# Optimization experiments

Hardware: AMD Instinct MI355X
Metric: run time of the kernel (lower is better)

The kernel has to match this reference:

```python
import jax, jax.numpy as jnp
import numpy as np

B = 8          # number of scenes in batch
N_PER = 4096   # points per scene (equal-sized contiguous batches)
C_IN = 64
C_OUT = 128
RATIO = 0.25
K = 32
EPS = 1e-5


def setup_inputs() -> dict:
    key = jax.random.key(0)
    ks = jax.random.split(key, 10)
    N = B * N_PER
    x = jax.random.normal(ks[0], (N, C_IN), dtype=jnp.float32)
    pos = jax.random.uniform(ks[1], (N, 3), dtype=jnp.float32)
    batch = jnp.repeat(jnp.arange(B, dtype=jnp.int64), N_PER)
    d_in = C_IN + 3
    s1 = 1.0 / np.sqrt(d_in)
    s2 = 1.0 / np.sqrt(C_OUT)
    W1 = jax.random.uniform(ks[2], (d_in, C_OUT), jnp.float32, -s1, s1)
    b1 = jax.random.uniform(ks[3], (C_OUT,), jnp.float32, -s1, s1)
    g1 = jnp.ones((C_OUT,), jnp.float32)
    be1 = jnp.zeros((C_OUT,), jnp.float32)
    W2 = jax.random.uniform(ks[4], (C_OUT, C_OUT), jnp.float32, -s2, s2)
    b2 = jax.random.uniform(ks[5], (C_OUT,), jnp.float32, -s2, s2)
    g2 = jnp.ones((C_OUT,), jnp.float32)
    be2 = jnp.zeros((C_OUT,), jnp.float32)
    return {"x": x, "pos": pos, "batch": batch, "W1": W1, "b1": b1,
            "g1": g1, "be1": be1, "W2": W2, "b2": b2, "g2": g2, "be2": be2}


def _ln(y, g, b):
    mu = y.mean(-1, keepdims=True)
    v = ((y - mu) ** 2).mean(-1, keepdims=True)
    return (y - mu) * jax.lax.rsqrt(v + EPS) * g + b


def reference(x, pos, batch, W1, b1, g1, be1, W2, b2, g2, be2):
    N, C = x.shape
    n = N_PER
    m = int(n * RATIO)  # samples per scene
    xb = x.reshape(B, n, C)
    posb = pos.reshape(B, n, 3)
    # deterministic sampling: first m points of each (randomly generated) scene
    pos_down = posb[:, :m]  # (B, m, 3)
    # squared euclidean distances (same ordering as cdist for topk/argmin)
    d2 = jnp.sum((pos_down[:, :, None, :] - posb[:, None, :, :]) ** 2, axis=-1)  # (B,m,n)
    _, knn_idx = jax.lax.top_k(-d2, K)  # (B, m, K), k smallest distances
    bidx = jnp.arange(B)[:, None, None]
    knn_feat = xb[bidx, knn_idx]       # (B, m, K, C)
    knn_pos = posb[bidx, knn_idx]      # (B, m, K, 3)
    rel_pos = knn_pos - pos_down[:, :, None, :]
    h = jnp.concatenate([knn_feat, rel_pos], axis=-1)  # (B, m, K, C+3)
    h = jax.nn.gelu(_ln(h @ W1 + b1, g1, be1), approximate=False)
    h = jax.nn.gelu(_ln(h @ W2 + b2, g2, be2), approximate=False)
    x_down = h.max(axis=2).reshape(B * m, -1)          # (M, C_OUT)
    pos_down_flat = pos_down.reshape(B * m, 3)
    batch_down = jnp.repeat(jnp.arange(B, dtype=batch.dtype), m)
    # nearest downsampled point for each original point (for upsampling)
    d2u = jnp.sum((posb[:, :, None, :] - pos_down[:, None, :, :]) ** 2, axis=-1)  # (B,n,m)
    nearest = jnp.argmin(d2u, axis=-1)                 # (B, n), local index
    upsample_idx = (nearest + jnp.arange(B)[:, None] * m).reshape(N)
    return x_down, pos_down_flat, batch_down, upsample_idx
```

## Files before the change

### kernel.cpp

```cpp
#include <hip/hip_runtime.h>
#include <math.h>

#define NPER 4096
#define MDOWN 1024
#define KNNK 32
#define CIN 64
#define DIN 67
#define KPAD 96
#define SSTR 136

typedef _Float16 half8 __attribute__((ext_vector_type(8)));
typedef _Float16 half4 __attribute__((ext_vector_type(4)));
typedef float f32x4 __attribute__((ext_vector_type(4)));

#define SENTU 0xFFFFFFFFFFFFFFFFULL

__device__ __forceinline__ float d2f(float qx, float qy, float qz,
                                     float px, float py, float pz) {
    float dx = __fsub_rn(qx, px);
    float dy = __fsub_rn(qy, py);
    float dz = __fsub_rn(qz, pz);
    return __fadd_rn(__fadd_rn(__fmul_rn(dx, dx), __fmul_rn(dy, dy)), __fmul_rn(dz, dz));
}

__device__ __forceinline__ float gelu_f(float y) {
    return 0.5f * y * (1.0f + erff(y * 0.70710678118654752440f));
}

__device__ __forceinline__ void insert4(unsigned long long v,
                                        unsigned long long& t0, unsigned long long& t1,
                                        unsigned long long& t2, unsigned long long& t3) {
    if (v < t3) {
        unsigned long long m2 = t2 > v ? t2 : v;
        t3 = t3 < m2 ? t3 : m2;
        unsigned long long m1 = t1 > v ? t1 : v;
        t2 = t2 < m1 ? t2 : m1;
        unsigned long long m0 = t0 > v ? t0 : v;
        t1 = t1 < m0 ? t1 : m0;
        t0 = t0 < v ? t0 : v;
    }
}

__global__ __launch_bounds__(256) void prep_kernel(const float* __restrict__ W1,
                                                   const float* __restrict__ W2,
                                                   _Float16* __restrict__ W1t,
                                                   _Float16* __restrict__ W2t) {
    int t = blockIdx.x * 256 + threadIdx.x;
    if (t < 128 * KPAD) {
        int k = t >> 7, c = t & 127;
        float v = (k < DIN) ? W1[k * 128 + c] : 0.0f;
        W1t[(size_t)c * KPAD + k] = (_Float16)v;
    }
    int t2 = t - 128 * KPAD;
    if (t2 >= 0 && t2 < 128 * 128) {
        int k = t2 >> 7, c = t2 & 127;
        W2t[(size_t)c * 128 + k] = (_Float16)W2[t2];
    }
}

__global__ __launch_bounds__(256) void knn_kernel(const float* __restrict__ pos,
                                                  int* __restrict__ knn) {
    int tid = threadIdx.x;
    int lane = tid & 63;
    int q = blockIdx.x * 4 + (tid >> 6);
    int b = q >> 10;
    int i = q & 1023;
    const float* pb = pos + (size_t)b * NPER * 3;
    float qx = pb[i * 3], qy = pb[i * 3 + 1], qz = pb[i * 3 + 2];

    unsigned long long t0 = SENTU, t1 = SENTU, t2 = SENTU, t3 = SENTU;
    unsigned long long taken = 0ULL;

    #pragma unroll 4
    for (int s = 0; s < 64; ++s) {
        int j = s * 64 + lane;
        float d2 = d2f(qx, qy, qz, pb[j * 3], pb[j * 3 + 1], pb[j * 3 + 2]);
        unsigned long long v = ((unsigned long long)__float_as_uint(d2) << 32) | (unsigned)j;
        insert4(v, t0, t1, t2, t3);
    }

    for (int r = 0; r < KNNK; ++r) {
        if (t0 == SENTU) {
            for (int s = 0; s < 64; ++s) {
                if (!((taken >> s) & 1ULL)) {
                    int j = s * 64 + lane;
                    float d2 = d2f(qx, qy, qz, pb[j * 3], pb[j * 3 + 1], pb[j * 3 + 2]);
                    unsigned long long v =
                        ((unsigned long long)__float_as_uint(d2) << 32) | (unsigned)j;
                    insert4(v, t0, t1, t2, t3);
                }
            }
        }
        unsigned long long w = t0;
        #pragma unroll
        for (int d = 1; d < 64; d <<= 1) {
            unsigned long long o = __shfl_xor(w, d, 64);
            w = o < w ? o : w;
        }
        if (t0 == w) {
            taken |= 1ULL << (((unsigned)(w & 0xFFFFFFFFu)) >> 6);
            t0 = t1; t1 = t2; t2 = t3; t3 = SENTU;
        }
        if (lane == 0) knn[q * KNNK + r] = (int)(unsigned)(w & 0xFFFFFFFFu);
    }
}

__global__ __launch_bounds__(512, 4) void mlp_kernel(
    const float* __restrict__ x, const float* __restrict__ pos,
    const int* __restrict__ knn,
    const _Float16* __restrict__ W1t, const _Float16* __restrict__ W2t,
    const float* __restrict__ b1, const float* __restrict__ g1, const float* __restrict__ be1,
    const float* __restrict__ b2, const float* __restrict__ g2, const float* __restrict__ be2,
    float* __restrict__ out0) {
    __shared__ __align__(16) _Float16 S[128][SSTR];
    __shared__ float pmax[8][128];
    __shared__ int jidx[128];
    __shared__ float qpos[4][3];

    int tid = threadIdx.x;
    int q0 = blockIdx.x * 4;
    int b = q0 >> 10;
    const float* pb = pos + (size_t)b * NPER * 3;

    if (tid < 128) jidx[tid] = knn[(q0 + (tid >> 5)) * KNNK + (tid & 31)];
    if (tid < 12) {
        int qq = tid / 3, comp = tid % 3;
        int iq = (q0 + qq) & 1023;
        qpos[qq][comp] = pb[iq * 3 + comp];
    }
    __syncthreads();

    for (int t = tid; t < 128 * 16; t += 512) {
        int r = t >> 4, c4 = (t & 15) * 4;
        int j = jidx[r];
        float4 v = *(const float4*)(x + ((size_t)(b * NPER + j)) * CIN + c4);
        half4 hv = {(_Float16)v.x, (_Float16)v.y, (_Float16)v.z, (_Float16)v.w};
        *(half4*)&S[r][c4] = hv;
    }
    for (int t = tid; t < 128 * 8; t += 512) {
        int r = t >> 3, k = t & 7;
        half4 hv = {(_Float16)0.f, (_Float16)0.f, (_Float16)0.f, (_Float16)0.f};
        if (k == 0) {
            int j = jidx[r];
            int qq = r >> 5;
            hv.x = (_Float16)__fsub_rn(pb[j * 3 + 0], qpos[qq][0]);
            hv.y = (_Float16)__fsub_rn(pb[j * 3 + 1], qpos[qq][1]);
            hv.z = (_Float16)__fsub_rn(pb[j * 3 + 2], qpos[qq][2]);
        }
        *(half4*)&S[r][64 + 4 * k] = hv;
    }
    __syncthreads();

    int lane = tid & 63, wid = tid >> 6;
    int c16 = lane & 15, g = lane >> 4;
    int r0 = wid * 16;

    f32x4 acc[8];
    #pragma unroll
    for (int n = 0; n < 8; ++n) acc[n] = (f32x4){0.f, 0.f, 0.f, 0.f};

    #pragma unroll
    for (int ks = 0; ks < 3; ++ks) {
        half8 a = *(const half8*)&S[r0 + c16][ks * 32 + 8 * g];
        #pragma unroll
        for (int n = 0; n < 8; ++n) {
            half8 bf = *(const half8*)(W1t + (size_t)(n * 16 + c16) * KPAD + ks * 32 + 8 * g);
            acc[n] = __builtin_amdgcn_mfma_f32_16x16x32_f16(a, bf, acc[n], 0, 0, 0);
        }
    }

    {
        float bv[8], gv[8], bev[8];
        #pragma unroll
        for (int n = 0; n < 8; ++n) {
            int c = n * 16 + c16;
            bv[n] = b1[c]; gv[n] = g1[c]; bev[n] = be1[c];
        }
        #pragma unroll
        for (int t = 0; t < 4; ++t) {
            float s = 0.f;
            #pragma unroll
            for (int n = 0; n < 8; ++n) { acc[n][t] += bv[n]; s += acc[n][t]; }
            s += __shfl_xor(s, 1, 64); s += __shfl_xor(s, 2, 64);
            s += __shfl_xor(s, 4, 64); s += __shfl_xor(s, 8, 64);
            float mu = s * (1.0f / 128.0f);
            float vv = 0.f;
            #pragma unroll
            for (int n = 0; n < 8; ++n) { float d = acc[n][t] - mu; vv += d * d; }
            vv += __shfl_xor(vv, 1, 64); vv += __shfl_xor(vv, 2, 64);
            vv += __shfl_xor(vv, 4, 64); vv += __shfl_xor(vv, 8, 64);
            float rstd = rsqrtf(vv * (1.0f / 128.0f) + 1e-5f);
            int row = r0 + 4 * g + t;
            #pragma unroll
            for (int n = 0; n < 8; ++n) {
                float z = (acc[n][t] - mu) * rstd;
                float y = z * gv[n] + bev[n];
                S[row][16 * n + c16] = (_Float16)gelu_f(y);
            }
        }
    }

    f32x4 acc2[8];
    #pragma unroll
    for (int n = 0; n < 8; ++n) acc2[n] = (f32x4){0.f, 0.f, 0.f, 0.f};

    #pragma unroll
    for (int ks = 0; ks < 4; ++ks) {
        half8 a = *(const half8*)&S[r0 + c16][ks * 32 + 8 * g];
        #pragma unroll
        for (int n = 0; n < 8; ++n) {
            half8 bf = *(const half8*)(W2t + (size_t)(n * 16 + c16) * 128 + ks * 32 + 8 * g);
            acc2[n] = __builtin_amdgcn_mfma_f32_16x16x32_f16(a, bf, acc2[n], 0, 0, 0);
        }
    }

    {
        float bv[8], gv[8], bev[8];
        #pragma unroll
        for (int n = 0; n < 8; ++n) {
            int c = n * 16 + c16;
            bv[n] = b2[c]; gv[n] = g2[c]; bev[n] = be2[c];
        }
        float mx[8];
        #pragma unroll
        for (int n = 0; n < 8; ++n) mx[n] = -3.4e38f;
        #pragma unroll
        for (int t = 0; t < 4; ++t) {
            float s = 0.f;
            #pragma unroll
            for (int n = 0; n < 8; ++n) { acc2[n][t] += bv[n]; s += acc2[n][t]; }
            s += __shfl_xor(s, 1, 64); s += __shfl_xor(s, 2, 64);
            s += __shfl_xor(s, 4, 64); s += __shfl_xor(s, 8, 64);
            float mu = s * (1.0f / 128.0f);
            float vv = 0.f;
            #pragma unroll
            for (int n = 0; n < 8; ++n) { float d = acc2[n][t] - mu; vv += d * d; }
            vv += __shfl_xor(vv, 1, 64); vv += __shfl_xor(vv, 2, 64);
            vv += __shfl_xor(vv, 4, 64); vv += __shfl_xor(vv, 8, 64);
            float rstd = rsqrtf(vv * (1.0f / 128.0f) + 1e-5f);
            #pragma unroll
            for (int n = 0; n < 8; ++n) {
                float z = (acc2[n][t] - mu) * rstd;
                float y = z * gv[n] + bev[n];
                float h = gelu_f(y);
                mx[n] = fmaxf(mx[n], h);
            }
        }
        #pragma unroll
        for (int n = 0; n < 8; ++n) {
            mx[n] = fmaxf(mx[n], __shfl_xor(mx[n], 16, 64));
            mx[n] = fmaxf(mx[n], __shfl_xor(mx[n], 32, 64));
        }
        if (lane < 16) {
            #pragma unroll
            for (int n = 0; n < 8; ++n) pmax[wid][n * 16 + c16] = mx[n];
        }
    }
    __syncthreads();

    {
        int q = tid >> 7, c = tid & 127;
        out0[(size_t)(q0 + q) * 128 + c] = fmaxf(pmax[2 * q][c], pmax[2 * q + 1][c]);
    }
}

__global__ __launch_bounds__(256) void up_kernel(const float* __restrict__ pos,
                                                 float* __restrict__ out1,
                                                 float* __restrict__ out2,
                                                 float* __restrict__ out3) {
    int b = blockIdx.x >> 6, jb = blockIdx.x & 63;
    __shared__ float pd[3072];
    __shared__ unsigned long long red[192];
    int tid = threadIdx.x;
    const float* pb = pos + (size_t)b * NPER * 3;
    for (int t = tid; t < 3072; t += 256) pd[t] = pb[t];
    __syncthreads();

    int qlane = tid & 63;
    int part = tid >> 6;
    int j = jb * 64 + qlane;
    float qx = pb[j * 3], qy = pb[j * 3 + 1], qz = pb[j * 3 + 2];
    unsigned long long best = SENTU;
    int i0 = part * 256;
    #pragma unroll 4
    for (int i = i0; i < i0 + 256; ++i) {
        float d2 = d2f(qx, qy, qz, pd[i * 3], pd[i * 3 + 1], pd[i * 3 + 2]);
        unsigned long long v = ((unsigned long long)__float_as_uint(d2) << 32) | (unsigned)i;
        best = v < best ? v : best;
    }
    if (part > 0) red[(part - 1) * 64 + qlane] = best;
    __syncthreads();
    if (part == 0) {
        unsigned long long o0 = red[qlane];
        unsigned long long o1 = red[64 + qlane];
        unsigned long long o2 = red[128 + qlane];
        best = o0 < best ? o0 : best;
        best = o1 < best ? o1 : best;
        best = o2 < best ? o2 : best;
        int ii = (int)(unsigned)(best & 0xFFFFFFFFu);
        out3[(size_t)b * NPER + j] = (float)(ii + b * MDOWN);
    }
    if (jb == 0) {
        for (int t = tid; t < 3072; t += 256) out1[b * 3072 + t] = pd[t];
        for (int t = tid; t < 1024; t += 256) out2[b * 1024 + t] = (float)b;
    }
}

extern "C" void kernel_launch(void* const* d_in, const int* in_sizes, int n_in,
                              void* d_out, int out_size, void* d_ws, size_t ws_size,
                              hipStream_t stream) {
    const float* x   = (const float*)d_in[0];
    const float* pos = (const float*)d_in[1];
    const float* W1  = (const float*)d_in[3];
    const float* b1  = (const float*)d_in[4];
    const float* g1  = (const float*)d_in[5];
    const float* be1 = (const float*)d_in[6];
    const float* W2  = (const float*)d_in[7];
    const float* b2  = (const float*)d_in[8];
    const float* g2  = (const float*)d_in[9];
    const float* be2 = (const float*)d_in[10];

    float* out  = (float*)d_out;
    float* out0 = out;
    float* out1 = out + 1048576;
    float* out2 = out + 1048576 + 24576;
    float* out3 = out + 1048576 + 24576 + 8192;

    int* knn = (int*)d_ws;
    _Float16* W1t = (_Float16*)((char*)d_ws + 8192 * 32 * 4);
    _Float16* W2t = W1t + 128 * KPAD;

    prep_kernel<<<112, 256, 0, stream>>>(W1, W2, W1t, W2t);
    knn_kernel<<<2048, 256, 0, stream>>>(pos, knn);
    mlp_kernel<<<2048, 512, 0, stream>>>(x, pos, knn, W1t, W2t,
                                         b1, g1, be1, b2, g2, be2, out0);
    up_kernel<<<512, 256, 0, stream>>>(pos, out1, out2, out3);
}
```

Baseline: 295.9 us.

## Apply GELU only at neighbour min/max and use polynomial erf approximation

Because GELU is unimodal (decreasing then increasing), the max over neighbours of GELU(y) equals the larger of GELU at the min and max of y. The second layer now tracks per-channel min/max of the pre-activation and evaluates GELU twice per output instead of per neighbour. Separately, erff is replaced by an Abramowitz–Stegun rational approximation with fast exp, cheapening the first layer's GELU at a small accuracy cost. An extra shared array and more shuffles are added for the min tracking.

```diff
diff --git a/kernel.cpp b/kernel.cpp
--- a/kernel.cpp
+++ b/kernel.cpp
@@ -24,7 +24,18 @@
 }
 
 __device__ __forceinline__ float gelu_f(float y) {
-    return 0.5f * y * (1.0f + erff(y * 0.70710678118654752440f));
+    float x = y * 0.70710678118654752440f;
+    float ax = fabsf(x);
+    float t = __frcp_rn(__fmaf_rn(0.3275911f, ax, 1.0f));
+    float p = __fmaf_rn(1.061405429f, t, -1.453152027f);
+    p = __fmaf_rn(p, t, 1.421413741f);
+    p = __fmaf_rn(p, t, -0.284496736f);
+    p = __fmaf_rn(p, t, 0.254829592f);
+    p = p * t;
+    float e = __expf(-ax * ax);
+    float erfax = __fmaf_rn(-p, e, 1.0f);
+    float er = copysignf(erfax, x);
+    return 0.5f * y * (1.0f + er);
 }
 
 __device__ __forceinline__ void insert4(unsigned long long v,
@@ -113,7 +124,8 @@
     const float* __restrict__ b2, const float* __restrict__ g2, const float* __restrict__ be2,
     float* __restrict__ out0) {
     __shared__ __align__(16) _Float16 S[128][SSTR];
-    __shared__ float pmax[8][128];
+    __shared__ float pymx[8][128];
+    __shared__ float pymn[8][128];
     __shared__ int jidx[128];
     __shared__ float qpos[4][3];
 
@@ -221,9 +233,9 @@
             int c = n * 16 + c16;
             bv[n] = b2[c]; gv[n] = g2[c]; bev[n] = be2[c];
         }
-        float mx[8];
-        #pragma unroll
-        for (int n = 0; n < 8; ++n) mx[n] = -3.4e38f;
+        float ymx[8], ymn[8];
+        #pragma unroll
+        for (int n = 0; n < 8; ++n) { ymx[n] = -3.4e38f; ymn[n] = 3.4e38f; }
         #pragma unroll
         for (int t = 0; t < 4; ++t) {
             float s = 0.f;
@@ -242,25 +254,32 @@
             for (int n = 0; n < 8; ++n) {
                 float z = (acc2[n][t] - mu) * rstd;
                 float y = z * gv[n] + bev[n];
-                float h = gelu_f(y);
-                mx[n] = fmaxf(mx[n], h);
+                ymx[n] = fmaxf(ymx[n], y);
+                ymn[n] = fminf(ymn[n], y);
             }
         }
         #pragma unroll
         for (int n = 0; n < 8; ++n) {
-            mx[n] = fmaxf(mx[n], __shfl_xor(mx[n], 16, 64));
-            mx[n] = fmaxf(mx[n], __shfl_xor(mx[n], 32, 64));
+            ymx[n] = fmaxf(ymx[n], __shfl_xor(ymx[n], 16, 64));
+            ymx[n] = fmaxf(ymx[n], __shfl_xor(ymx[n], 32, 64));
+            ymn[n] = fminf(ymn[n], __shfl_xor(ymn[n], 16, 64));
+            ymn[n] = fminf(ymn[n], __shfl_xor(ymn[n], 32, 64));
         }
         if (lane < 16) {
             #pragma unroll
-            for (int n = 0; n < 8; ++n) pmax[wid][n * 16 + c16] = mx[n];
+            for (int n = 0; n < 8; ++n) {
+                pymx[wid][n * 16 + c16] = ymx[n];
+                pymn[wid][n * 16 + c16] = ymn[n];
+            }
         }
     }
     __syncthreads();
 
     {
         int q = tid >> 7, c = tid & 127;
-        out0[(size_t)(q0 + q) * 128 + c] = fmaxf(pmax[2 * q][c], pmax[2 * q + 1][c]);
+        float y1 = fmaxf(pymx[2 * q][c], pymx[2 * q + 1][c]);
+        float y0 = fminf(pymn[2 * q][c], pymn[2 * q + 1][c]);
+        out0[(size_t)(q0 + q) * 128 + c] = fmaxf(gelu_f(y0), gelu_f(y1));
     }
 }
 
```

Result: faster. 282.3 us (-4.6%).
